# Kernel optimization log

Measured on AMD Instinct MI355X. Metric: run time of the kernel, lower is better.

The kernel has to match this reference:

```python
import jax, jax.numpy as jnp
import numpy as np

HEADS = 16
HEAD_DIM = 128
K = 128  # sparsek_k; k_actual = min(K, seq_len) = K here


def _sparsek_impl(scores):
    # scores: [B, H, S]; sparsemax-like projection with mass k
    n = scores.shape[-1]
    s = -jnp.sort(-scores, axis=-1)                      # descending sort
    cs = jnp.cumsum(s, axis=-1)
    ar = jnp.arange(1, n + 1, dtype=scores.dtype)
    thr = (cs - float(K)) / ar
    support = s > thr
    rho = jnp.clip(support.sum(axis=-1, keepdims=True), 1, None)  # int
    tau = (jnp.take_along_axis(cs, rho - 1, axis=-1) - float(K)) / rho.astype(scores.dtype)
    return jnp.clip(scores - tau, 0.0, None)


@jax.custom_vjp
def sparsek(scores):
    return _sparsek_impl(scores)


def _sparsek_fwd(scores):
    out = _sparsek_impl(scores)
    return out, (out,)


def _sparsek_bwd(res, g):
    (out,) = res
    support = (out > 0).astype(g.dtype)
    ns = jnp.clip(support.sum(axis=-1, keepdims=True), 1.0, None)
    grad = support * (g - (g * support).sum(axis=-1, keepdims=True) / ns)
    return (grad,)


sparsek.defvjp(_sparsek_fwd, _sparsek_bwd)


def setup_inputs() -> dict:
    key = jax.random.key(0)
    ks = jax.random.split(key, 9)
    B, S, H = 2, 4096, 2048
    sc = 0.02
    return {
        "x": jax.random.normal(ks[0], (B, S, H), jnp.float32),
        "wq": jax.random.normal(ks[1], (H, H), jnp.float32) * sc,
        "wk": jax.random.normal(ks[2], (H, H), jnp.float32) * sc,
        "wv": jax.random.normal(ks[3], (H, H), jnp.float32) * sc,
        "wo": jax.random.normal(ks[4], (H, H), jnp.float32) * sc,
        "sw1": jax.random.normal(ks[5], (HEAD_DIM, HEAD_DIM), jnp.float32) * sc,
        "sb1": jnp.zeros((HEAD_DIM,), jnp.float32),
        "sw2": jax.random.normal(ks[6], (1, HEAD_DIM), jnp.float32) * sc,
        "sb2": jnp.zeros((1,), jnp.float32),
    }


def reference(x, wq, wk, wv, wo, sw1, sb1, sw2, sb2):
    B, S, H = x.shape
    scale = 1.0 / np.sqrt(HEAD_DIM)

    def split_heads(y):  # [B,S,H] -> [B,heads,S,head_dim]
        return y.reshape(B, S, HEADS, HEAD_DIM).transpose(0, 2, 1, 3)

    q = split_heads(x @ wq.T)
    k = split_heads(x @ wk.T)
    v = split_heads(x @ wv.T)

    # score_net: Linear -> ReLU -> Linear(.,1), applied to keys
    kv_scores = (jax.nn.relu(k @ sw1.T + sb1) @ sw2.T + sb2)[..., 0]  # [B,heads,S]
    selection = sparsek(kv_scores)
    _, top_idx = jax.lax.top_k(selection, K)  # [B,heads,K]

    idx = top_idx[..., None]  # [B,heads,K,1]
    k_sel = jnp.take_along_axis(k, idx, axis=2)  # [B,heads,K,head_dim]
    v_sel = jnp.take_along_axis(v, idx, axis=2)

    scores = jnp.einsum('bhqd,bhkd->bhqk', q, k_sel) * scale
    attn = jax.nn.softmax(scores, axis=-1)  # dropout p=0 (eval)
    out = jnp.einsum('bhqk,bhkd->bhqd', attn, v_sel)
    out = out.transpose(0, 2, 1, 3).reshape(B, S, H)
    return out @ wo.T
```

## Files before the change

### kernel.cpp

```cpp
#include <hip/hip_runtime.h>

#define SEQ   4096
#define NB    2
#define NH    16
#define HD    128
#define TOPK  128
#define MDIM  (NB*SEQ)
#define NDIM  2048
#define KDIM  2048

typedef unsigned short u16;
typedef __bf16  v8bf __attribute__((ext_vector_type(8)));
typedef float   v4f  __attribute__((ext_vector_type(4)));

__device__ __forceinline__ u16 f2b(float f) {
    unsigned u = __float_as_uint(f);
    return (u16)((u + 0x7fffu + ((u >> 16) & 1u)) >> 16);
}
__device__ __forceinline__ float b2f(u16 h) {
    return __uint_as_float(((unsigned)h) << 16);
}

#define ASYNC16(gsrc, ldst) \
    __builtin_amdgcn_global_load_lds( \
        (const __attribute__((address_space(1))) unsigned int*)(gsrc), \
        (__attribute__((address_space(3))) unsigned int*)(ldst), 16, 0, 0)

__global__ __launch_bounds__(256) void split_f32(const float* __restrict__ in,
                                                 u16* __restrict__ hi,
                                                 u16* __restrict__ lo, long n)
{
    long i = ((long)blockIdx.x * 256 + threadIdx.x) * 4;
    if (i >= n) return;
    float4 v = *(const float4*)(in + i);
    float vv[4] = {v.x, v.y, v.z, v.w};
    u16 h[4], l[4];
#pragma unroll
    for (int j = 0; j < 4; ++j) {
        h[j] = f2b(vv[j]);
        l[j] = f2b(vv[j] - b2f(h[j]));
    }
    uint2 ph, pl;
    ph.x = (unsigned)h[0] | ((unsigned)h[1] << 16);
    ph.y = (unsigned)h[2] | ((unsigned)h[3] << 16);
    pl.x = (unsigned)l[0] | ((unsigned)l[1] << 16);
    pl.y = (unsigned)l[2] | ((unsigned)l[3] << 16);
    *(uint2*)(hi + i) = ph;
    *(uint2*)(lo + i) = pl;
}

__global__ __launch_bounds__(256) void cvt_bf16(const float* __restrict__ in,
                                                u16* __restrict__ outb, long n)
{
    long i = ((long)blockIdx.x * 256 + threadIdx.x) * 4;
    if (i >= n) return;
    float4 v = *(const float4*)(in + i);
    uint2 p;
    p.x = (unsigned)f2b(v.x) | ((unsigned)f2b(v.y) << 16);
    p.y = (unsigned)f2b(v.z) | ((unsigned)f2b(v.w) << 16);
    *(uint2*)(outb + i) = p;
}

#define GM_STORE_F32 0
#define GM_ACC_F32   1
#define GM_STORE_B16 2

#define BAR    __builtin_amdgcn_s_barrier()
#define LGK0   do { asm volatile("s_waitcnt lgkmcnt(0)" ::: "memory"); \
                    __builtin_amdgcn_sched_barrier(0); } while (0)
#define VMW(n) asm volatile("s_waitcnt vmcnt(" #n ")" ::: "memory")

__global__ __launch_bounds__(512, 2) void gemm256(const u16* __restrict__ A,
                                                  const u16* __restrict__ W,
                                                  float* __restrict__ Cf,
                                                  u16* __restrict__ Cb,
                                                  int mode)
{
    __shared__ __attribute__((aligned(16))) u16 S[65536];

    const int t    = threadIdx.x;
    const int swz  = (blockIdx.x & 7) * 32 + (blockIdx.x >> 3);
    const int bm   = swz >> 3, bn = swz & 7;
    const int lane = t & 63;
    const int wm   = (t >> 6) >> 2, wn = (t >> 6) & 3;
    const int mr   = lane & 15, q4 = lane >> 4;

    const int rA  = t >> 3;
    const int cc8 = ((t & 7) ^ (rA & 7)) * 8;
    const int rB  = (t >> 8) * 64 + (rA & 31);
    const u16* Agp = A + (long)(bm * 256 + rA) * KDIM + cc8;
    const u16* Wgp = W + (long)(bn * 256 + rB) * KDIM + cc8;
    u16* ldA = S +         rA * 64 + (t & 7) * 8;
    u16* ldB = S + 32768 + rB * 64 + (t & 7) * 8;

#define STAGE_A(kt, i) do { \
        const u16* g_ = Agp + (long)(i) * 64 * KDIM + (kt) * 64; \
        u16* d_ = ldA + ((kt) & 1) * 16384 + (i) * 4096; \
        ASYNC16(g_, d_); ASYNC16(g_ + 128 * KDIM, d_ + 8192); \
    } while (0)
#define STAGE_B(kt, j) do { \
        const u16* g_ = Wgp + (long)(j) * 32 * KDIM + (kt) * 64; \
        u16* d_ = ldB + ((kt) & 1) * 16384 + (j) * 2048; \
        ASYNC16(g_, d_); ASYNC16(g_ + 128 * KDIM, d_ + 8192); \
    } while (0)

    v4f acc[8][4];
#pragma unroll
    for (int a = 0; a < 8; ++a)
#pragma unroll
        for (int c = 0; c < 4; ++c)
            acc[a][c] = (v4f){0.f, 0.f, 0.f, 0.f};

    v8bf aF[4][2], bF[2][2][2];
#define LDA(b, i) do { \
        _Pragma("unroll") for (int mt = 0; mt < 4; ++mt) { \
            const int r_ = wm * 128 + (i) * 64 + mt * 16 + mr; \
            _Pragma("unroll") for (int ks = 0; ks < 2; ++ks) \
                aF[mt][ks] = *(const v8bf*)&S[(b) * 16384 + r_ * 64 + \
                                    (((ks * 4 + q4) ^ (r_ & 7)) * 8)]; \
        } } while (0)
#define LDB(b, j) do { \
        _Pragma("unroll") for (int nt = 0; nt < 2; ++nt) { \
            const int r_ = wn * 64 + (j) * 32 + nt * 16 + mr; \
            _Pragma("unroll") for (int ks = 0; ks < 2; ++ks) \
                bF[j][nt][ks] = *(const v8bf*)&S[32768 + (b) * 16384 + r_ * 64 + \
                                    (((ks * 4 + q4) ^ (r_ & 7)) * 8)]; \
        } } while (0)
#define MMA(i, j) do { \
        __builtin_amdgcn_s_setprio(1); \
        _Pragma("unroll") for (int mt = 0; mt < 4; ++mt) \
        _Pragma("unroll") for (int nt = 0; nt < 2; ++nt) \
        _Pragma("unroll") for (int ks = 0; ks < 2; ++ks) \
            acc[(i) * 4 + mt][(j) * 2 + nt] = \
                __builtin_amdgcn_mfma_f32_16x16x32_bf16(aF[mt][ks], bF[j][nt][ks], \
                    acc[(i) * 4 + mt][(j) * 2 + nt], 0, 0, 0); \
        __builtin_amdgcn_s_setprio(0); \
    } while (0)

    STAGE_A(0, 0); STAGE_B(0, 0); STAGE_A(0, 1); STAGE_B(0, 1);
    STAGE_A(1, 0); STAGE_B(1, 0);
    VMW(4); BAR;

    for (int it = 0; it < KDIM / 128 - 1; ++it) {
        const int T = 2 * it;
        LDA(0, 0); LDB(0, 0); STAGE_A(T + 1, 1);          BAR; LGK0; MMA(0, 0); BAR;
        LDB(0, 1);            STAGE_B(T + 1, 1);          BAR; LGK0; MMA(0, 1); BAR;
        LDA(0, 1);            STAGE_A(T + 2, 0);          BAR; LGK0; MMA(1, 0); BAR;
                              STAGE_B(T + 2, 0); VMW(4);  BAR;       MMA(1, 1); BAR;
        LDA(1, 0); LDB(1, 0); STAGE_A(T + 2, 1);          BAR; LGK0; MMA(0, 0); BAR;
        LDB(1, 1);            STAGE_B(T + 2, 1);          BAR; LGK0; MMA(0, 1); BAR;
        LDA(1, 1);            STAGE_A(T + 3, 0);          BAR; LGK0; MMA(1, 0); BAR;
                              STAGE_B(T + 3, 0); VMW(4);  BAR;       MMA(1, 1); BAR;
    }
    LDA(0, 0); LDB(0, 0); STAGE_A(31, 1);                 BAR; LGK0; MMA(0, 0); BAR;
    LDB(0, 1);            STAGE_B(31, 1);                 BAR; LGK0; MMA(0, 1); BAR;
    LDA(0, 1);                                            BAR; LGK0; MMA(1, 0); BAR;
                                             VMW(0);      BAR;       MMA(1, 1); BAR;
    LDA(1, 0); LDB(1, 0);                                 BAR; LGK0; MMA(0, 0); BAR;
    LDB(1, 1);                                            BAR; LGK0; MMA(0, 1); BAR;
    LDA(1, 1);                                            BAR; LGK0; MMA(1, 0); BAR;
                                                                     MMA(1, 1);

    const int colb = bn * 256 + wn * 64 + mr;
    const int rowb = bm * 256 + wm * 128 + q4 * 4;
#pragma unroll
    for (int a = 0; a < 8; ++a) {
        const int ro = (a >> 2) * 64 + (a & 3) * 16;
#pragma unroll
        for (int r = 0; r < 4; ++r) {
            const long base = (long)(rowb + ro + r) * NDIM + colb;
#pragma unroll
            for (int c = 0; c < 4; ++c) {
                const float v = acc[a][c][r];
                const long off = base + (c >> 1) * 32 + (c & 1) * 16;
                if (mode == GM_STORE_F32)      Cf[off] = v;
                else if (mode == GM_ACC_F32)   Cf[off] += v;
                else                           Cb[off] = f2b(v);
            }
        }
    }
#undef STAGE_A
#undef STAGE_B
#undef LDA
#undef LDB
#undef MMA
}

__global__ __launch_bounds__(256) void scorenet(const float* __restrict__ Kb,
                                                const float* __restrict__ sw1,
                                                const float* __restrict__ sb1,
                                                const float* __restrict__ sw2,
                                                const float* __restrict__ sb2,
                                                float* __restrict__ scores)
{
    __shared__ float As[16][128];
    __shared__ float Bs[16][128];
    __shared__ float red[128][17];
    const int t  = threadIdx.x;
    const int tx = t & 15, ty = t >> 4;
    const int bm = blockIdx.x;
    const int lr = t >> 1;
    const int lc = (t & 1) * 8;
    const float* Ap = Kb + (long)(bm * 128 + lr) * HD + lc;
    const float* Wp = sw1 + lr * HD + lc;

    float acc[8][8];
#pragma unroll
    for (int i = 0; i < 8; ++i)
#pragma unroll
        for (int j = 0; j < 8; ++j) acc[i][j] = 0.f;

    for (int k0 = 0; k0 < HD; k0 += 16) {
        float4 a0 = *(const float4*)(Ap + k0);
        float4 a1 = *(const float4*)(Ap + k0 + 4);
        float4 b0 = *(const float4*)(Wp + k0);
        float4 b1 = *(const float4*)(Wp + k0 + 4);
        __syncthreads();
        As[lc+0][lr] = a0.x; As[lc+1][lr] = a0.y; As[lc+2][lr] = a0.z; As[lc+3][lr] = a0.w;
        As[lc+4][lr] = a1.x; As[lc+5][lr] = a1.y; As[lc+6][lr] = a1.z; As[lc+7][lr] = a1.w;
        Bs[lc+0][lr] = b0.x; Bs[lc+1][lr] = b0.y; Bs[lc+2][lr] = b0.z; Bs[lc+3][lr] = b0.w;
        Bs[lc+4][lr] = b1.x; Bs[lc+5][lr] = b1.y; Bs[lc+6][lr] = b1.z; Bs[lc+7][lr] = b1.w;
        __syncthreads();
#pragma unroll
        for (int kk = 0; kk < 16; ++kk) {
            float a[8], b[8];
            *(float4*)&a[0] = *(const float4*)&As[kk][ty * 8];
            *(float4*)&a[4] = *(const float4*)&As[kk][ty * 8 + 4];
            *(float4*)&b[0] = *(const float4*)&Bs[kk][tx * 8];
            *(float4*)&b[4] = *(const float4*)&Bs[kk][tx * 8 + 4];
#pragma unroll
            for (int i = 0; i < 8; ++i)
#pragma unroll
                for (int j = 0; j < 8; ++j)
                    acc[i][j] = fmaf(a[i], b[j], acc[i][j]);
        }
    }

    float b1v[8], w2v[8];
#pragma unroll
    for (int j = 0; j < 8; ++j) {
        b1v[j] = sb1[tx * 8 + j];
        w2v[j] = sw2[tx * 8 + j];
    }
#pragma unroll
    for (int i = 0; i < 8; ++i) {
        float p = 0.f;
#pragma unroll
        for (int j = 0; j < 8; ++j)
            p += fmaxf(acc[i][j] + b1v[j], 0.f) * w2v[j];
        red[ty * 8 + i][tx] = p;
    }
    __syncthreads();
    if (t < 128) {
        float s = sb2[0];
#pragma unroll
        for (int c = 0; c < 16; ++c) s += red[t][c];
        long r = (long)bm * 128 + t;
        int b  = (int)(r >> 16);
        int si = (int)((r >> 4) & (SEQ - 1));
        int h  = (int)(r & (NH - 1));
        scores[((b * NH + h) << 12) + si] = s;
    }
}

__global__ __launch_bounds__(256) void topk_sel(const float* __restrict__ scores,
                                                int* __restrict__ sel)
{
    __shared__ unsigned keys[SEQ];
    __shared__ unsigned hist[256];
    __shared__ int scal2[2];
    __shared__ unsigned cntG;
    __shared__ unsigned short tpre[256];
    const int t  = threadIdx.x;
    const int bh = blockIdx.x;
    const float* sc = scores + (long)bh * SEQ;
    for (int i = t; i < SEQ; i += 256) {
        unsigned u = __float_as_uint(sc[i]);
        u = (u & 0x80000000u) ? ~u : (u | 0x80000000u);
        keys[i] = u;
    }
    unsigned prefix = 0;
    int rem = TOPK;
    const int i0 = t * 16;
    for (int shift = 24; shift >= 0; shift -= 8) {
        hist[t] = 0;
        __syncthreads();
        const unsigned pm = (shift == 24) ? 0u : (0xFFFFFFFFu << (shift + 8));
        for (int i = i0; i < i0 + 16; ++i) {
            unsigned k = keys[i];
            if (((k ^ prefix) & pm) == 0) atomicAdd(&hist[(k >> shift) & 255], 1u);
        }
        __syncthreads();
        if (t == 0) {
            int r = rem, chosen = 0;
            for (int b = 255; b >= 0; --b) {
                int c = (int)hist[b];
                if (c >= r) { chosen = b; break; }
                r -= c;
            }
            scal2[0] = chosen; scal2[1] = r;
        }
        __syncthreads();
        prefix |= ((unsigned)scal2[0]) << shift;
        rem = scal2[1];
        __syncthreads();
    }
    if (t == 0) cntG = 0;
    __syncthreads();
    const unsigned T = prefix;
    int myT = 0;
    for (int i = i0; i < i0 + 16; ++i) {
        unsigned k = keys[i];
        if (k > T) {
            unsigned p = atomicAdd(&cntG, 1u);
            sel[bh * TOPK + p] = i;
        } else if (k == T) myT++;
    }
    tpre[t] = (unsigned short)myT;
    __syncthreads();
    if (t == 0) {
        unsigned s = 0;
        for (int i = 0; i < 256; ++i) { unsigned c = tpre[i]; tpre[i] = (unsigned short)s; s += c; }
    }
    __syncthreads();
    const int base = TOPK - rem;
    int rank = tpre[t];
    for (int i = i0; i < i0 + 16; ++i) {
        if (keys[i] == T) {
            if (rank < rem) sel[bh * TOPK + base + rank] = i;
            rank++;
        }
    }
}

__global__ void gather_kv(const float* __restrict__ Kf, const u16* __restrict__ Vb,
                          const int* __restrict__ sel,
                          u16* __restrict__ ksb, u16* __restrict__ vsT)
{
    int bh = blockIdx.x >> 7;
    int j  = blockIdx.x & 127;
    int d  = threadIdx.x;
    int s  = sel[bh * TOPK + j];
    int b = bh >> 4, h = bh & (NH - 1);
    long src = ((long)(b * SEQ + s)) * NDIM + h * HD + d;
    ksb[((long)bh * TOPK + j) * HD + d] = f2b(Kf[src]);
    vsT[((long)bh * HD + d) * TOPK + j] = Vb[src];
}

__device__ __forceinline__ int paddr(int row, int col) {
    int chunk = (col >> 3) ^ (row & 15);
    return row * 128 + chunk * 8 + (col & 7);
}

__global__ __launch_bounds__(256) void attn_mfma(const u16* __restrict__ Qb,
                                                 const u16* __restrict__ ksb,
                                                 const u16* __restrict__ vsT,
                                                 u16* __restrict__ outp)
{
    __shared__ __attribute__((aligned(16))) u16 P[128 * 128];
    const int bh = blockIdx.x, qt = blockIdx.y;
    const int b = bh >> 4, h = bh & (NH - 1);
    const int t = threadIdx.x, lane = t & 63, w = t >> 6;
    const int mr = lane & 15, q4 = lane >> 4;
    const float scale = 0.08838834764831845f;

    const u16* q0p = Qb + ((long)(b * SEQ + qt * 128 + w * 32 + mr)) * NDIM
                        + h * HD + q4 * 8;
    v8bf aq[2][4];
#pragma unroll
    for (int ks = 0; ks < 4; ++ks) {
        aq[0][ks] = *(const v8bf*)(q0p + ks * 32);
        aq[1][ks] = *(const v8bf*)(q0p + 16 * NDIM + ks * 32);
    }

    const u16* kbase = ksb + (long)bh * TOPK * HD + mr * HD + q4 * 8;
    v4f acc[2][8];
#pragma unroll
    for (int i = 0; i < 2; ++i)
#pragma unroll
        for (int j = 0; j < 8; ++j) {
            acc[i][j][0] = 0.f; acc[i][j][1] = 0.f;
            acc[i][j][2] = 0.f; acc[i][j][3] = 0.f;
        }
#pragma unroll
    for (int ks = 0; ks < 4; ++ks) {
        v8bf bk[8];
#pragma unroll
        for (int nt = 0; nt < 8; ++nt)
            bk[nt] = *(const v8bf*)(kbase + (long)nt * 16 * HD + ks * 32);
#pragma unroll
        for (int mt = 0; mt < 2; ++mt)
#pragma unroll
            for (int nt = 0; nt < 8; ++nt)
                acc[mt][nt] = __builtin_amdgcn_mfma_f32_16x16x32_bf16(
                                  aq[mt][ks], bk[nt], acc[mt][nt], 0, 0, 0);
    }

#pragma unroll
    for (int mt = 0; mt < 2; ++mt)
#pragma unroll
        for (int r = 0; r < 4; ++r) {
            float mx = acc[mt][0][r];
#pragma unroll
            for (int nt = 1; nt < 8; ++nt) mx = fmaxf(mx, acc[mt][nt][r]);
#pragma unroll
            for (int m = 1; m < 16; m <<= 1) mx = fmaxf(mx, __shfl_xor(mx, m));
            float sum = 0.f;
#pragma unroll
            for (int nt = 0; nt < 8; ++nt) {
                float e = __expf((acc[mt][nt][r] - mx) * scale);
                acc[mt][nt][r] = e; sum += e;
            }
#pragma unroll
            for (int m = 1; m < 16; m <<= 1) sum += __shfl_xor(sum, m);
            float inv = 1.f / sum;
#pragma unroll
            for (int nt = 0; nt < 8; ++nt) acc[mt][nt][r] *= inv;
        }

#pragma unroll
    for (int mt = 0; mt < 2; ++mt)
#pragma unroll
        for (int nt = 0; nt < 8; ++nt)
#pragma unroll
            for (int r = 0; r < 4; ++r)
                P[paddr(w * 32 + mt * 16 + q4 * 4 + r, nt * 16 + mr)] =
                    f2b(acc[mt][nt][r]);
    __syncthreads();

    const u16* vbase = vsT + (long)bh * HD * TOPK + mr * TOPK + q4 * 8;
    v4f acc2[2][8];
#pragma unroll
    for (int i = 0; i < 2; ++i)
#pragma unroll
        for (int j = 0; j < 8; ++j) {
            acc2[i][j][0] = 0.f; acc2[i][j][1] = 0.f;
            acc2[i][j][2] = 0.f; acc2[i][j][3] = 0.f;
        }
#pragma unroll
    for (int ks = 0; ks < 4; ++ks) {
        v8bf ap[2];
        ap[0] = *(const v8bf*)&P[paddr(w * 32 + mr,      ks * 32 + q4 * 8)];
        ap[1] = *(const v8bf*)&P[paddr(w * 32 + 16 + mr, ks * 32 + q4 * 8)];
        v8bf bv[8];
#pragma unroll
        for (int nt = 0; nt < 8; ++nt)
            bv[nt] = *(const v8bf*)(vbase + (long)nt * 16 * TOPK + ks * 32);
#pragma unroll
        for (int mt = 0; mt < 2; ++mt)
#pragma unroll
            for (int nt = 0; nt < 8; ++nt)
                acc2[mt][nt] = __builtin_amdgcn_mfma_f32_16x16x32_bf16(
                                   ap[mt], bv[nt], acc2[mt][nt], 0, 0, 0);
    }
    __syncthreads();

#pragma unroll
    for (int mt = 0; mt < 2; ++mt)
#pragma unroll
        for (int nt = 0; nt < 8; ++nt)
#pragma unroll
            for (int r = 0; r < 4; ++r)
                P[paddr(w * 32 + mt * 16 + q4 * 4 + r, nt * 16 + mr)] =
                    f2b(acc2[mt][nt][r]);
    __syncthreads();

    u16* obase = outp + ((long)(b * SEQ + qt * 128)) * NDIM + h * HD;
    for (int f = t; f < 2048; f += 256) {
        int row = f >> 4, cc = f & 15;
        uint4 val = *(const uint4*)&P[row * 128 + (cc ^ (row & 15)) * 8];
        *(uint4*)(obase + (long)row * NDIM + cc * 8) = val;
    }
}

extern "C" void kernel_launch(void* const* d_in, const int* in_sizes, int n_in,
                              void* d_out, int out_size, void* d_ws, size_t ws_size,
                              hipStream_t stream)
{
    const float* x   = (const float*)d_in[0];
    const float* wq  = (const float*)d_in[1];
    const float* wk  = (const float*)d_in[2];
    const float* wv  = (const float*)d_in[3];
    const float* wo  = (const float*)d_in[4];
    const float* sw1 = (const float*)d_in[5];
    const float* sb1 = (const float*)d_in[6];
    const float* sw2 = (const float*)d_in[7];
    const float* sb2 = (const float*)d_in[8];
    float* out = (float*)d_out;

    char* base = (char*)d_ws;
    u16*   xh      = (u16*)  base;
    u16*   xl      = (u16*) (base + 33554432L);
    float* Kf      = (float*)(base + 67108864L);
    u16*   Vb      = (u16*) (base + 134217728L);
    u16*   W1      = (u16*) (base + 167772160L);
    u16*   W2      = (u16*) (base + 176160768L);
    float* scoresB = (float*)(base + 184549376L);
    int*   sel     = (int*) (base + 185073664L);
    u16*   ksb     = (u16*) (base + 185090048L);
    u16*   vsT     = (u16*) (base + 186138624L);
    u16*   Qb      = xl;
    u16*   AOb     = Vb;

    const long NX = (long)MDIM * NDIM;
    dim3 blk(256);
    const int g256 = (MDIM / 256) * (NDIM / 256);

    split_f32<<<16384, blk, 0, stream>>>(x,  xh, xl, NX);
    split_f32<<<4096,  blk, 0, stream>>>(wk, W1, W2, (long)NDIM * KDIM);
    gemm256<<<g256, 512, 0, stream>>>(xh, W1, Kf, nullptr, GM_STORE_F32);
    gemm256<<<g256, 512, 0, stream>>>(xh, W2, Kf, nullptr, GM_ACC_F32);
    gemm256<<<g256, 512, 0, stream>>>(xl, W1, Kf, nullptr, GM_ACC_F32);
    cvt_bf16<<<4096, blk, 0, stream>>>(wq, W1, (long)NDIM * KDIM);
    cvt_bf16<<<4096, blk, 0, stream>>>(wv, W2, (long)NDIM * KDIM);
    gemm256<<<g256, 512, 0, stream>>>(xh, W1, nullptr, Qb, GM_STORE_B16);
    gemm256<<<g256, 512, 0, stream>>>(xh, W2, nullptr, Vb, GM_STORE_B16);
    scorenet<<<(MDIM * NH) / 128, blk, 0, stream>>>(Kf, sw1, sb1, sw2, sb2, scoresB);
    topk_sel<<<NB * NH, blk, 0, stream>>>(scoresB, sel);
    gather_kv<<<NB * NH * TOPK, 128, 0, stream>>>(Kf, Vb, sel, ksb, vsT);
    attn_mfma<<<dim3(NB * NH, SEQ / 128), blk, 0, stream>>>(Qb, ksb, vsT, AOb);
    cvt_bf16<<<4096, blk, 0, stream>>>(wo, W1, (long)NDIM * KDIM);
    gemm256<<<g256, 512, 0, stream>>>(AOb, W1, out, nullptr, GM_STORE_F32);
}
```

Before: 739.8 us.

## Fuse three split-bf16 K-projection GEMMs into one kernel; split LDS waits

```diff
diff --git a/kernel.cpp b/kernel.cpp
--- a/kernel.cpp
+++ b/kernel.cpp
@@ -26,6 +26,14 @@
         (const __attribute__((address_space(1))) unsigned int*)(gsrc), \
         (__attribute__((address_space(3))) unsigned int*)(ldst), 16, 0, 0)
 
+#define BAR     __builtin_amdgcn_s_barrier()
+#define SCB0    __builtin_amdgcn_sched_barrier(0)
+#define SP1     __builtin_amdgcn_s_setprio(1)
+#define SP0     __builtin_amdgcn_s_setprio(0)
+#define LGKC(n) do { asm volatile("s_waitcnt lgkmcnt(" #n ")" ::: "memory"); \
+                     __builtin_amdgcn_sched_barrier(0); } while (0)
+#define VMW(n)  asm volatile("s_waitcnt vmcnt(" #n ")" ::: "memory")
+
 __global__ __launch_bounds__(256) void split_f32(const float* __restrict__ in,
                                                  u16* __restrict__ hi,
                                                  u16* __restrict__ lo, long n)
@@ -64,11 +72,6 @@
 #define GM_STORE_F32 0
 #define GM_ACC_F32   1
 #define GM_STORE_B16 2
-
-#define BAR    __builtin_amdgcn_s_barrier()
-#define LGK0   do { asm volatile("s_waitcnt lgkmcnt(0)" ::: "memory"); \
-                    __builtin_amdgcn_sched_barrier(0); } while (0)
-#define VMW(n) asm volatile("s_waitcnt vmcnt(" #n ")" ::: "memory")
 
 __global__ __launch_bounds__(512, 2) void gemm256(const u16* __restrict__ A,
                                                   const u16* __restrict__ W,
@@ -112,29 +115,27 @@
             acc[a][c] = (v4f){0.f, 0.f, 0.f, 0.f};
 
     v8bf aF[4][2], bF[2][2][2];
-#define LDA(b, i) do { \
-        _Pragma("unroll") for (int mt = 0; mt < 4; ++mt) { \
-            const int r_ = wm * 128 + (i) * 64 + mt * 16 + mr; \
-            _Pragma("unroll") for (int ks = 0; ks < 2; ++ks) \
-                aF[mt][ks] = *(const v8bf*)&S[(b) * 16384 + r_ * 64 + \
-                                    (((ks * 4 + q4) ^ (r_ & 7)) * 8)]; \
-        } } while (0)
 #define LDB(b, j) do { \
         _Pragma("unroll") for (int nt = 0; nt < 2; ++nt) { \
             const int r_ = wn * 64 + (j) * 32 + nt * 16 + mr; \
             _Pragma("unroll") for (int ks = 0; ks < 2; ++ks) \
                 bF[j][nt][ks] = *(const v8bf*)&S[32768 + (b) * 16384 + r_ * 64 + \
                                     (((ks * 4 + q4) ^ (r_ & 7)) * 8)]; \
-        } } while (0)
-#define MMA(i, j) do { \
-        __builtin_amdgcn_s_setprio(1); \
-        _Pragma("unroll") for (int mt = 0; mt < 4; ++mt) \
+        } SCB0; } while (0)
+#define LDAH(b, i, h) do { \
+        _Pragma("unroll") for (int mt = 2*(h); mt < 2*(h)+2; ++mt) { \
+            const int r_ = wm * 128 + (i) * 64 + mt * 16 + mr; \
+            _Pragma("unroll") for (int ks = 0; ks < 2; ++ks) \
+                aF[mt][ks] = *(const v8bf*)&S[(b) * 16384 + r_ * 64 + \
+                                    (((ks * 4 + q4) ^ (r_ & 7)) * 8)]; \
+        } SCB0; } while (0)
+#define MMAH(i, j, h) do { \
+        _Pragma("unroll") for (int mt = 2*(h); mt < 2*(h)+2; ++mt) \
         _Pragma("unroll") for (int nt = 0; nt < 2; ++nt) \
         _Pragma("unroll") for (int ks = 0; ks < 2; ++ks) \
             acc[(i) * 4 + mt][(j) * 2 + nt] = \
-                __builtin_amdgcn_mfma_f32_16x16x32_bf16(aF[mt][ks], bF[j][nt][ks], \
+                __builtin_amdgcn_mfma_f32_16x16x32_bf16(aF[mt][ks], bF[(j)][nt][ks], \
                     acc[(i) * 4 + mt][(j) * 2 + nt], 0, 0, 0); \
-        __builtin_amdgcn_s_setprio(0); \
     } while (0)
 
     STAGE_A(0, 0); STAGE_B(0, 0); STAGE_A(0, 1); STAGE_B(0, 1);
@@ -143,23 +144,38 @@
 
     for (int it = 0; it < KDIM / 128 - 1; ++it) {
         const int T = 2 * it;
-        LDA(0, 0); LDB(0, 0); STAGE_A(T + 1, 1);          BAR; LGK0; MMA(0, 0); BAR;
-        LDB(0, 1);            STAGE_B(T + 1, 1);          BAR; LGK0; MMA(0, 1); BAR;
-        LDA(0, 1);            STAGE_A(T + 2, 0);          BAR; LGK0; MMA(1, 0); BAR;
-                              STAGE_B(T + 2, 0); VMW(4);  BAR;       MMA(1, 1); BAR;
-        LDA(1, 0); LDB(1, 0); STAGE_A(T + 2, 1);          BAR; LGK0; MMA(0, 0); BAR;
-        LDB(1, 1);            STAGE_B(T + 2, 1);          BAR; LGK0; MMA(0, 1); BAR;
-        LDA(1, 1);            STAGE_A(T + 3, 0);          BAR; LGK0; MMA(1, 0); BAR;
-                              STAGE_B(T + 3, 0); VMW(4);  BAR;       MMA(1, 1); BAR;
-    }
-    LDA(0, 0); LDB(0, 0); STAGE_A(31, 1);                 BAR; LGK0; MMA(0, 0); BAR;
-    LDB(0, 1);            STAGE_B(31, 1);                 BAR; LGK0; MMA(0, 1); BAR;
-    LDA(0, 1);                                            BAR; LGK0; MMA(1, 0); BAR;
-                                             VMW(0);      BAR;       MMA(1, 1); BAR;
-    LDA(1, 0); LDB(1, 0);                                 BAR; LGK0; MMA(0, 0); BAR;
-    LDB(1, 1);                                            BAR; LGK0; MMA(0, 1); BAR;
-    LDA(1, 1);                                            BAR; LGK0; MMA(1, 0); BAR;
-                                                                     MMA(1, 1);
+        LDB(0,0); LDAH(0,0,0); LDAH(0,0,1); STAGE_A(T+1,1);
+        BAR; LGKC(4); SP1; MMAH(0,0,0); LGKC(0); MMAH(0,0,1); SP0; BAR;
+        LDB(0,1); STAGE_B(T+1,1);
+        BAR; LGKC(0); SP1; MMAH(0,1,0); MMAH(0,1,1); SP0; BAR;
+        LDAH(0,1,0); LDAH(0,1,1); STAGE_A(T+2,0);
+        BAR; LGKC(4); SP1; MMAH(1,0,0); LGKC(0); MMAH(1,0,1); SP0; BAR;
+        STAGE_B(T+2,0); VMW(4);
+        BAR; SP1; MMAH(1,1,0); MMAH(1,1,1); SP0; BAR;
+        LDB(1,0); LDAH(1,0,0); LDAH(1,0,1); STAGE_A(T+2,1);
+        BAR; LGKC(4); SP1; MMAH(0,0,0); LGKC(0); MMAH(0,0,1); SP0; BAR;
+        LDB(1,1); STAGE_B(T+2,1);
+        BAR; LGKC(0); SP1; MMAH(0,1,0); MMAH(0,1,1); SP0; BAR;
+        LDAH(1,1,0); LDAH(1,1,1); STAGE_A(T+3,0);
+        BAR; LGKC(4); SP1; MMAH(1,0,0); LGKC(0); MMAH(1,0,1); SP0; BAR;
+        STAGE_B(T+3,0); VMW(4);
+        BAR; SP1; MMAH(1,1,0); MMAH(1,1,1); SP0; BAR;
+    }
+    LDB(0,0); LDAH(0,0,0); LDAH(0,0,1); STAGE_A(31,1);
+    BAR; LGKC(4); SP1; MMAH(0,0,0); LGKC(0); MMAH(0,0,1); SP0; BAR;
+    LDB(0,1); STAGE_B(31,1);
+    BAR; LGKC(0); SP1; MMAH(0,1,0); MMAH(0,1,1); SP0; BAR;
+    LDAH(0,1,0); LDAH(0,1,1);
+    BAR; LGKC(4); SP1; MMAH(1,0,0); LGKC(0); MMAH(1,0,1); SP0; BAR;
+    VMW(0);
+    BAR; SP1; MMAH(1,1,0); MMAH(1,1,1); SP0; BAR;
+    LDB(1,0); LDAH(1,0,0); LDAH(1,0,1);
+    BAR; LGKC(4); SP1; MMAH(0,0,0); LGKC(0); MMAH(0,0,1); SP0; BAR;
+    LDB(1,1);
+    BAR; LGKC(0); SP1; MMAH(0,1,0); MMAH(0,1,1); SP0; BAR;
+    LDAH(1,1,0); LDAH(1,1,1);
+    BAR; LGKC(4); SP1; MMAH(1,0,0); LGKC(0); MMAH(1,0,1); SP0; BAR;
+    SP1; MMAH(1,1,0); MMAH(1,1,1); SP0;
 
     const int colb = bn * 256 + wn * 64 + mr;
     const int rowb = bm * 256 + wm * 128 + q4 * 4;
@@ -181,9 +197,125 @@
     }
 #undef STAGE_A
 #undef STAGE_B
-#undef LDA
 #undef LDB
-#undef MMA
+#undef LDAH
+#undef MMAH
+}
+
+__global__ __launch_bounds__(512, 2) void gemm_k3(const u16* __restrict__ Ah,
+                                                  const u16* __restrict__ Al,
+                                                  const u16* __restrict__ W1,
+                                                  const u16* __restrict__ W2,
+                                                  float* __restrict__ Cf)
+{
+    __shared__ __attribute__((aligned(16))) u16 S[65536];
+
+    const int t    = threadIdx.x;
+    const int swz  = (blockIdx.x & 7) * 32 + (blockIdx.x >> 3);
+    const int bm   = swz >> 3, bn = swz & 7;
+    const int lane = t & 63;
+    const int wm   = (t >> 6) >> 2, wn = (t >> 6) & 3;
+    const int mr   = lane & 15, q4 = lane >> 4;
+    const int ck   = q4 ^ ((mr ^ (mr >> 2)) & 3);
+
+    const int lr    = t >> 2;
+    const int cks   = (t & 3) ^ ((lr ^ (lr >> 2)) & 3);
+    const int growA = (lr & 63) + ((lr & 64) << 1);
+    const int growB = (lr & 31) + ((lr >> 5) << 6);
+    const u16* Ahp = Ah + (long)(bm * 256 + growA) * KDIM + cks * 8;
+    const u16* Alp = Al + (long)(bm * 256 + growA) * KDIM + cks * 8;
+    const u16* W1p = W1 + (long)(bn * 256 + growB) * KDIM + cks * 8;
+    const u16* W2p = W2 + (long)(bn * 256 + growB) * KDIM + cks * 8;
+    u16* dA = S +         lr * 32 + (t & 3) * 8;
+    u16* dB = S + 16384 + lr * 32 + (t & 3) * 8;
+
+#define K3SA(kt, s) do { \
+        const long g_ = (long)(s) * 64 * KDIM + (kt) * 32; \
+        u16* d_ = dA + (((kt) & 1) << 15) + (s) * 8192; \
+        ASYNC16(Ahp + g_, d_); ASYNC16(Alp + g_, d_ + 4096); } while (0)
+#define K3SB(kt, s) do { \
+        const long g_ = (long)(s) * 32 * KDIM + (kt) * 32; \
+        u16* d_ = dB + (((kt) & 1) << 15) + (s) * 8192; \
+        ASYNC16(W1p + g_, d_); ASYNC16(W2p + g_, d_ + 4096); } while (0)
+
+    v4f acc[8][4];
+#pragma unroll
+    for (int a = 0; a < 8; ++a)
+#pragma unroll
+        for (int c = 0; c < 4; ++c)
+            acc[a][c] = (v4f){0.f, 0.f, 0.f, 0.f};
+
+    v8bf aFh[4], aFl[4], b1[2][2], b2[2][2];
+    const int aBase = wm * 2048 + mr * 32 + ck * 8;
+    const int bBase = 16384 + wn * 1024 + mr * 32 + ck * 8;
+
+#define K3RB(bb, j) do { \
+        _Pragma("unroll") for (int nt = 0; nt < 2; ++nt) { \
+            b1[j][nt] = *(const v8bf*)&S[(bb) + bBase + (j) * 8192 + nt * 512]; \
+            b2[j][nt] = *(const v8bf*)&S[(bb) + bBase + (j) * 8192 + nt * 512 + 4096]; \
+        } SCB0; } while (0)
+#define K3RAH(bb, i) do { _Pragma("unroll") for (int mt = 0; mt < 4; ++mt) \
+        aFh[mt] = *(const v8bf*)&S[(bb) + aBase + (i) * 8192 + mt * 512]; SCB0; } while (0)
+#define K3RAL(bb, i) do { _Pragma("unroll") for (int mt = 0; mt < 4; ++mt) \
+        aFl[mt] = *(const v8bf*)&S[(bb) + aBase + (i) * 8192 + mt * 512 + 4096]; SCB0; } while (0)
+#define K3CL(af, bx, i, j) do { \
+        _Pragma("unroll") for (int mt = 0; mt < 4; ++mt) \
+        _Pragma("unroll") for (int nt = 0; nt < 2; ++nt) \
+            acc[(i) * 4 + mt][(j) * 2 + nt] = __builtin_amdgcn_mfma_f32_16x16x32_bf16( \
+                af[mt], bx[(j)][nt], acc[(i) * 4 + mt][(j) * 2 + nt], 0, 0, 0); } while (0)
+
+    K3SA(0, 0); K3SB(0, 0); K3SB(0, 1); K3SA(0, 1);
+    VMW(4); BAR;
+
+    for (int T = 0; T < KDIM / 32 - 1; ++T) {
+        const int bb = (T & 1) << 15;
+        K3RB(bb, 0); K3RAH(bb, 0); K3RAL(bb, 0); K3SA(T + 1, 0);
+        BAR; LGKC(4); SP1; K3CL(aFh, b1, 0, 0); K3CL(aFh, b2, 0, 0);
+        LGKC(0); K3CL(aFl, b1, 0, 0); SP0; VMW(4); BAR;
+        K3RB(bb, 1); K3SB(T + 1, 0);
+        BAR; LGKC(0); SP1; K3CL(aFh, b1, 0, 1); K3CL(aFh, b2, 0, 1);
+        K3CL(aFl, b1, 0, 1); SP0; VMW(4); BAR;
+        K3RAH(bb, 1); K3RAL(bb, 1); K3SB(T + 1, 1);
+        BAR; LGKC(4); SP1; K3CL(aFh, b1, 1, 0); K3CL(aFh, b2, 1, 0);
+        LGKC(0); K3CL(aFl, b1, 1, 0); SP0; BAR;
+        K3SA(T + 1, 1);
+        BAR; SP1; K3CL(aFh, b1, 1, 1); K3CL(aFh, b2, 1, 1);
+        K3CL(aFl, b1, 1, 1); SP0; VMW(4); BAR;
+    }
+    {
+        const int bb = 32768;
+        K3RB(bb, 0); K3RAH(bb, 0); K3RAL(bb, 0);
+        BAR; LGKC(4); SP1; K3CL(aFh, b1, 0, 0); K3CL(aFh, b2, 0, 0);
+        LGKC(0); K3CL(aFl, b1, 0, 0); SP0; VMW(2); BAR;
+        K3RB(bb, 1);
+        BAR; LGKC(0); SP1; K3CL(aFh, b1, 0, 1); K3CL(aFh, b2, 0, 1);
+        K3CL(aFl, b1, 0, 1); SP0; VMW(0); BAR;
+        K3RAH(bb, 1); K3RAL(bb, 1);
+        BAR; LGKC(4); SP1; K3CL(aFh, b1, 1, 0); K3CL(aFh, b2, 1, 0);
+        LGKC(0); K3CL(aFl, b1, 1, 0); SP0; BAR;
+        SP1; K3CL(aFh, b1, 1, 1); K3CL(aFh, b2, 1, 1);
+        K3CL(aFl, b1, 1, 1); SP0;
+    }
+
+    const int colb = bn * 256 + wn * 64 + mr;
+    const int rowb = bm * 256 + wm * 128 + q4 * 4;
+#pragma unroll
+    for (int a = 0; a < 8; ++a) {
+        const int ro = (a >> 2) * 64 + (a & 3) * 16;
+#pragma unroll
+        for (int r = 0; r < 4; ++r) {
+            const long base = (long)(rowb + ro + r) * NDIM + colb;
+#pragma unroll
+            for (int c = 0; c < 4; ++c)
+                Cf[base + (c >> 1) * 32 + (c & 1) * 16] = acc[a][c][r];
+        }
+    }
+#undef K3SA
+#undef K3SB
+#undef K3RB
+#undef K3RAH
+#undef K3RAL
+#undef K3CL
 }
 
 __global__ __launch_bounds__(256) void scorenet(const float* __restrict__ Kb,
@@ -508,9 +640,7 @@
 
     split_f32<<<16384, blk, 0, stream>>>(x,  xh, xl, NX);
     split_f32<<<4096,  blk, 0, stream>>>(wk, W1, W2, (long)NDIM * KDIM);
-    gemm256<<<g256, 512, 0, stream>>>(xh, W1, Kf, nullptr, GM_STORE_F32);
-    gemm256<<<g256, 512, 0, stream>>>(xh, W2, Kf, nullptr, GM_ACC_F32);
-    gemm256<<<g256, 512, 0, stream>>>(xl, W1, Kf, nullptr, GM_ACC_F32);
+    gemm_k3<<<g256, 512, 0, stream>>>(xh, xl, W1, W2, Kf);
     cvt_bf16<<<4096, blk, 0, stream>>>(wq, W1, (long)NDIM * KDIM);
     cvt_bf16<<<4096, blk, 0, stream>>>(wv, W2, (long)NDIM * KDIM);
     gemm256<<<g256, 512, 0, stream>>>(xh, W1, nullptr, Qb, GM_STORE_B16);
```

New measurement: 667.0 us. 9.8% less time.

## Fuse three-pass split-bf16 K projection into one GEMM and repipeline gemm256

Applied to the files above, without the earlier changes.

```diff
diff --git a/kernel.cpp b/kernel.cpp
--- a/kernel.cpp
+++ b/kernel.cpp
@@ -26,6 +26,13 @@
         (const __attribute__((address_space(1))) unsigned int*)(gsrc), \
         (__attribute__((address_space(3))) unsigned int*)(ldst), 16, 0, 0)
 
+#define SCB0    __builtin_amdgcn_sched_barrier(0)
+#define BARS    do { __builtin_amdgcn_s_barrier(); SCB0; } while (0)
+#define SP1     __builtin_amdgcn_s_setprio(1)
+#define SP0     __builtin_amdgcn_s_setprio(0)
+#define LGKC(n) do { asm volatile("s_waitcnt lgkmcnt(" #n ")" ::: "memory"); SCB0; } while (0)
+#define VMW(n)  do { asm volatile("s_waitcnt vmcnt(" #n ")" ::: "memory"); SCB0; } while (0)
+
 __global__ __launch_bounds__(256) void split_f32(const float* __restrict__ in,
                                                  u16* __restrict__ hi,
                                                  u16* __restrict__ lo, long n)
@@ -65,11 +72,6 @@
 #define GM_ACC_F32   1
 #define GM_STORE_B16 2
 
-#define BAR    __builtin_amdgcn_s_barrier()
-#define LGK0   do { asm volatile("s_waitcnt lgkmcnt(0)" ::: "memory"); \
-                    __builtin_amdgcn_sched_barrier(0); } while (0)
-#define VMW(n) asm volatile("s_waitcnt vmcnt(" #n ")" ::: "memory")
-
 __global__ __launch_bounds__(512, 2) void gemm256(const u16* __restrict__ A,
                                                   const u16* __restrict__ W,
                                                   float* __restrict__ Cf,
@@ -84,6 +86,7 @@
     const int lane = t & 63;
     const int wm   = (t >> 6) >> 2, wn = (t >> 6) & 3;
     const int mr   = lane & 15, q4 = lane >> 4;
+    const int sl0  = (q4 ^ (mr & 7)) * 8, sl1 = sl0 ^ 32;
 
     const int rA  = t >> 3;
     const int cc8 = ((t & 7) ^ (rA & 7)) * 8;
@@ -93,16 +96,14 @@
     u16* ldA = S +         rA * 64 + (t & 7) * 8;
     u16* ldB = S + 32768 + rB * 64 + (t & 7) * 8;
 
-#define STAGE_A(kt, i) do { \
+#define STAGE_A(kt, i) { \
         const u16* g_ = Agp + (long)(i) * 64 * KDIM + (kt) * 64; \
         u16* d_ = ldA + ((kt) & 1) * 16384 + (i) * 4096; \
-        ASYNC16(g_, d_); ASYNC16(g_ + 128 * KDIM, d_ + 8192); \
-    } while (0)
-#define STAGE_B(kt, j) do { \
+        ASYNC16(g_, d_); ASYNC16(g_ + 128 * KDIM, d_ + 8192); }
+#define STAGE_B(kt, j) { \
         const u16* g_ = Wgp + (long)(j) * 32 * KDIM + (kt) * 64; \
         u16* d_ = ldB + ((kt) & 1) * 16384 + (j) * 2048; \
-        ASYNC16(g_, d_); ASYNC16(g_ + 128 * KDIM, d_ + 8192); \
-    } while (0)
+        ASYNC16(g_, d_); ASYNC16(g_ + 128 * KDIM, d_ + 8192); }
 
     v4f acc[8][4];
 #pragma unroll
@@ -111,55 +112,50 @@
         for (int c = 0; c < 4; ++c)
             acc[a][c] = (v4f){0.f, 0.f, 0.f, 0.f};
 
-    v8bf aF[4][2], bF[2][2][2];
-#define LDA(b, i) do { \
-        _Pragma("unroll") for (int mt = 0; mt < 4; ++mt) { \
-            const int r_ = wm * 128 + (i) * 64 + mt * 16 + mr; \
-            _Pragma("unroll") for (int ks = 0; ks < 2; ++ks) \
-                aF[mt][ks] = *(const v8bf*)&S[(b) * 16384 + r_ * 64 + \
-                                    (((ks * 4 + q4) ^ (r_ & 7)) * 8)]; \
-        } } while (0)
-#define LDB(b, j) do { \
-        _Pragma("unroll") for (int nt = 0; nt < 2; ++nt) { \
-            const int r_ = wn * 64 + (j) * 32 + nt * 16 + mr; \
-            _Pragma("unroll") for (int ks = 0; ks < 2; ++ks) \
-                bF[j][nt][ks] = *(const v8bf*)&S[32768 + (b) * 16384 + r_ * 64 + \
-                                    (((ks * 4 + q4) ^ (r_ & 7)) * 8)]; \
-        } } while (0)
-#define MMA(i, j) do { \
-        __builtin_amdgcn_s_setprio(1); \
+    v8bf Aa[4][2], Ab[4][2];
+    v8bf Ba[2][2], Bb[2][2];
+
+#define RD_A(dst, b, i) { _Pragma("unroll") for (int mt = 0; mt < 4; ++mt) { \
+        const int ro_ = (b) * 16384 + (wm * 128 + (i) * 64 + mt * 16 + mr) * 64; \
+        dst[mt][0] = *(const v8bf*)&S[ro_ + sl0]; \
+        dst[mt][1] = *(const v8bf*)&S[ro_ + sl1]; } }
+#define RD_B(dst, b, j) { _Pragma("unroll") for (int nt = 0; nt < 2; ++nt) { \
+        const int ro_ = 32768 + (b) * 16384 + (wn * 64 + (j) * 32 + nt * 16 + mr) * 64; \
+        dst[nt][0] = *(const v8bf*)&S[ro_ + sl0]; \
+        dst[nt][1] = *(const v8bf*)&S[ro_ + sl1]; } }
+#define MM(AH, il, BH, jl) { SP1; \
         _Pragma("unroll") for (int mt = 0; mt < 4; ++mt) \
         _Pragma("unroll") for (int nt = 0; nt < 2; ++nt) \
         _Pragma("unroll") for (int ks = 0; ks < 2; ++ks) \
-            acc[(i) * 4 + mt][(j) * 2 + nt] = \
-                __builtin_amdgcn_mfma_f32_16x16x32_bf16(aF[mt][ks], bF[j][nt][ks], \
-                    acc[(i) * 4 + mt][(j) * 2 + nt], 0, 0, 0); \
-        __builtin_amdgcn_s_setprio(0); \
-    } while (0)
-
-    STAGE_A(0, 0); STAGE_B(0, 0); STAGE_A(0, 1); STAGE_B(0, 1);
-    STAGE_A(1, 0); STAGE_B(1, 0);
-    VMW(4); BAR;
-
-    for (int it = 0; it < KDIM / 128 - 1; ++it) {
-        const int T = 2 * it;
-        LDA(0, 0); LDB(0, 0); STAGE_A(T + 1, 1);          BAR; LGK0; MMA(0, 0); BAR;
-        LDB(0, 1);            STAGE_B(T + 1, 1);          BAR; LGK0; MMA(0, 1); BAR;
-        LDA(0, 1);            STAGE_A(T + 2, 0);          BAR; LGK0; MMA(1, 0); BAR;
-                              STAGE_B(T + 2, 0); VMW(4);  BAR;       MMA(1, 1); BAR;
-        LDA(1, 0); LDB(1, 0); STAGE_A(T + 2, 1);          BAR; LGK0; MMA(0, 0); BAR;
-        LDB(1, 1);            STAGE_B(T + 2, 1);          BAR; LGK0; MMA(0, 1); BAR;
-        LDA(1, 1);            STAGE_A(T + 3, 0);          BAR; LGK0; MMA(1, 0); BAR;
-                              STAGE_B(T + 3, 0); VMW(4);  BAR;       MMA(1, 1); BAR;
-    }
-    LDA(0, 0); LDB(0, 0); STAGE_A(31, 1);                 BAR; LGK0; MMA(0, 0); BAR;
-    LDB(0, 1);            STAGE_B(31, 1);                 BAR; LGK0; MMA(0, 1); BAR;
-    LDA(0, 1);                                            BAR; LGK0; MMA(1, 0); BAR;
-                                             VMW(0);      BAR;       MMA(1, 1); BAR;
-    LDA(1, 0); LDB(1, 0);                                 BAR; LGK0; MMA(0, 0); BAR;
-    LDB(1, 1);                                            BAR; LGK0; MMA(0, 1); BAR;
-    LDA(1, 1);                                            BAR; LGK0; MMA(1, 0); BAR;
-                                                                     MMA(1, 1);
+            acc[4*(il)+mt][2*(jl)+nt] = __builtin_amdgcn_mfma_f32_16x16x32_bf16( \
+                AH[mt][ks], BH[nt][ks], acc[4*(il)+mt][2*(jl)+nt], 0, 0, 0); \
+        SP0; }
+
+#define G_EV(U) \
+    RD_B(Bb, 0, 1); RD_A(Ab, 0, 1); SCB0; LGKC(12); MM(Aa, 0, Ba, 0); BARS; \
+    STAGE_A((U)+2, 0); STAGE_B((U)+2, 0); SCB0; VMW(8); LGKC(8); MM(Aa, 0, Bb, 1); BARS; \
+    RD_A(Aa, 1, 0); SCB0; STAGE_B((U)+2, 1); LGKC(8); MM(Ab, 1, Bb, 1); BARS; \
+    RD_B(Bb, 1, 0); SCB0; STAGE_A((U)+2, 1); VMW(8); MM(Ab, 1, Ba, 0); BARS;
+#define G_OD(U) \
+    RD_B(Ba, 1, 1); RD_A(Ab, 1, 1); SCB0; LGKC(12); MM(Aa, 0, Bb, 0); BARS; \
+    STAGE_A((U)+2, 0); STAGE_B((U)+2, 0); SCB0; VMW(8); LGKC(8); MM(Aa, 0, Ba, 1); BARS; \
+    RD_A(Aa, 0, 0); SCB0; STAGE_B((U)+2, 1); LGKC(8); MM(Ab, 1, Ba, 1); BARS; \
+    RD_B(Ba, 0, 0); SCB0; STAGE_A((U)+2, 1); VMW(8); MM(Ab, 1, Bb, 0); BARS;
+
+    STAGE_A(0, 0); STAGE_B(0, 0); STAGE_B(0, 1); STAGE_A(0, 1);
+    STAGE_A(1, 0); STAGE_B(1, 0); STAGE_B(1, 1); STAGE_A(1, 1);
+    VMW(8); BARS;
+    RD_A(Aa, 0, 0); RD_B(Ba, 0, 0); SCB0;
+
+    for (int U = 0; U < KDIM / 64 - 2; U += 2) { G_EV(U); G_OD(U + 1); }
+    RD_B(Bb, 0, 1); RD_A(Ab, 0, 1); SCB0; LGKC(12); MM(Aa, 0, Ba, 0); BARS;
+    VMW(4); LGKC(8); MM(Aa, 0, Bb, 1); BARS;
+    RD_A(Aa, 1, 0); SCB0; LGKC(8); MM(Ab, 1, Bb, 1); BARS;
+    RD_B(Bb, 1, 0); SCB0; VMW(0); MM(Ab, 1, Ba, 0); BARS;
+    RD_B(Ba, 1, 1); RD_A(Ab, 1, 1); SCB0; LGKC(12); MM(Aa, 0, Bb, 0); BARS;
+    LGKC(8); MM(Aa, 0, Ba, 1); BARS;
+    LGKC(0); MM(Ab, 1, Ba, 1);
+    MM(Ab, 1, Bb, 0);
 
     const int colb = bn * 256 + wn * 64 + mr;
     const int rowb = bm * 256 + wm * 128 + q4 * 4;
@@ -181,9 +177,125 @@
     }
 #undef STAGE_A
 #undef STAGE_B
-#undef LDA
-#undef LDB
-#undef MMA
+#undef RD_A
+#undef RD_B
+#undef MM
+#undef G_EV
+#undef G_OD
+}
+
+__global__ __launch_bounds__(512, 2) void gemm_k3(const u16* __restrict__ Ah,
+                                                  const u16* __restrict__ Al,
+                                                  const u16* __restrict__ W1,
+                                                  const u16* __restrict__ W2,
+                                                  float* __restrict__ Cf)
+{
+    __shared__ __attribute__((aligned(16))) u16 S[65536];
+
+    const int t    = threadIdx.x;
+    const int swz  = (blockIdx.x & 7) * 32 + (blockIdx.x >> 3);
+    const int bm   = swz >> 3, bn = swz & 7;
+    const int lane = t & 63;
+    const int wm   = (t >> 6) >> 2, wn = (t >> 6) & 3;
+    const int mr   = lane & 15, q4 = lane >> 4;
+    const int sl0  = (q4 ^ (mr & 7)) * 8, sl1 = sl0 ^ 32;
+    const int rlB0 = (wn & 1) * 32 + (wn >> 1) * 64 + mr;
+
+    const int lsl  = (t & 7) ^ ((t >> 3) & 7);
+    const int cS   = (lsl & 3) * 8;
+    const u16* baseA = ((lsl < 4) ? Ah : Al)
+                     + (long)(bm * 256 + (t >> 3)) * KDIM + cS;
+    const u16* baseB = ((lsl < 4) ? W1 : W2)
+                     + (long)(bn * 256 + (t >> 8) * 64 + ((t >> 3) & 31)) * KDIM + cS;
+    u16* dA = S +         t * 8;
+    u16* dB = S + 32768 + t * 8;
+
+#define K_SA(kt, si) { \
+        ASYNC16(baseA + ((long)(si) * 64      ) * KDIM + (kt) * 32, \
+                dA + (((kt) & 1) << 14) + (si) * 8192); \
+        ASYNC16(baseA + ((long)(si) * 64 + 128) * KDIM + (kt) * 32, \
+                dA + (((kt) & 1) << 14) + (si) * 8192 + 4096); }
+#define K_SB(kt, si) { \
+        ASYNC16(baseB + ((long)(si) * 32      ) * KDIM + (kt) * 32, \
+                dB + (((kt) & 1) << 14) + (si) * 8192); \
+        ASYNC16(baseB + ((long)(si) * 32 + 128) * KDIM + (kt) * 32, \
+                dB + (((kt) & 1) << 14) + (si) * 8192 + 4096); }
+
+    v4f acc[8][4];
+#pragma unroll
+    for (int a = 0; a < 8; ++a)
+#pragma unroll
+        for (int c = 0; c < 4; ++c)
+            acc[a][c] = (v4f){0.f, 0.f, 0.f, 0.f};
+
+    v8bf Ha[4], La[4], Hb[4], Lb[4];
+    v8bf B1a[2], B2a[2], B1b[2], B2b[2];
+
+#define K_RDA(dh, dl, b, i) { _Pragma("unroll") for (int mt = 0; mt < 4; ++mt) { \
+        const int ad = (b) * 16384 + (i) * 8192 + (mt * 16 + wm * 64 + mr) * 64; \
+        dh[mt] = *(const v8bf*)&S[ad + sl0]; \
+        dl[mt] = *(const v8bf*)&S[ad + sl1]; } }
+#define K_RDB(d1, d2, b, j) { _Pragma("unroll") for (int u = 0; u < 2; ++u) { \
+        const int ad = 32768 + (b) * 16384 + (j) * 8192 + (u * 16 + rlB0) * 64; \
+        d1[u] = *(const v8bf*)&S[ad + sl0]; \
+        d2[u] = *(const v8bf*)&S[ad + sl1]; } }
+#define K_MM(H, L, il, Bx, By, jl) { SP1; \
+        _Pragma("unroll") for (int mt = 0; mt < 4; ++mt) \
+        _Pragma("unroll") for (int u = 0; u < 2; ++u) { \
+            acc[4*(il)+mt][2*(jl)+u] = __builtin_amdgcn_mfma_f32_16x16x32_bf16( \
+                H[mt], Bx[u], acc[4*(il)+mt][2*(jl)+u], 0, 0, 0); \
+            acc[4*(il)+mt][2*(jl)+u] = __builtin_amdgcn_mfma_f32_16x16x32_bf16( \
+                H[mt], By[u], acc[4*(il)+mt][2*(jl)+u], 0, 0, 0); \
+            acc[4*(il)+mt][2*(jl)+u] = __builtin_amdgcn_mfma_f32_16x16x32_bf16( \
+                L[mt], Bx[u], acc[4*(il)+mt][2*(jl)+u], 0, 0, 0); } \
+        SP0; }
+
+#define K_EV(U) \
+    K_RDB(B1b, B2b, 0, 1); K_RDA(Hb, Lb, 0, 1); SCB0; LGKC(12); K_MM(Ha, La, 0, B1a, B2a, 0); BARS; \
+    K_SA((U)+2, 0); K_SB((U)+2, 0); SCB0; VMW(8); LGKC(8); K_MM(Ha, La, 0, B1b, B2b, 1); BARS; \
+    K_RDA(Ha, La, 1, 0); SCB0; K_SB((U)+2, 1); LGKC(8); K_MM(Hb, Lb, 1, B1b, B2b, 1); BARS; \
+    K_RDB(B1b, B2b, 1, 0); SCB0; K_SA((U)+2, 1); VMW(8); K_MM(Hb, Lb, 1, B1a, B2a, 0); BARS;
+#define K_OD(U) \
+    K_RDB(B1a, B2a, 1, 1); K_RDA(Hb, Lb, 1, 1); SCB0; LGKC(12); K_MM(Ha, La, 0, B1b, B2b, 0); BARS; \
+    K_SA((U)+2, 0); K_SB((U)+2, 0); SCB0; VMW(8); LGKC(8); K_MM(Ha, La, 0, B1a, B2a, 1); BARS; \
+    K_RDA(Ha, La, 0, 0); SCB0; K_SB((U)+2, 1); LGKC(8); K_MM(Hb, Lb, 1, B1a, B2a, 1); BARS; \
+    K_RDB(B1a, B2a, 0, 0); SCB0; K_SA((U)+2, 1); VMW(8); K_MM(Hb, Lb, 1, B1b, B2b, 0); BARS;
+
+    K_SA(0, 0); K_SB(0, 0); K_SB(0, 1); K_SA(0, 1);
+    K_SA(1, 0); K_SB(1, 0); K_SB(1, 1); K_SA(1, 1);
+    VMW(8); BARS;
+    K_RDA(Ha, La, 0, 0); K_RDB(B1a, B2a, 0, 0); SCB0;
+
+    for (int U = 0; U < KDIM / 32 - 2; U += 2) { K_EV(U); K_OD(U + 1); }
+    K_RDB(B1b, B2b, 0, 1); K_RDA(Hb, Lb, 0, 1); SCB0; LGKC(12); K_MM(Ha, La, 0, B1a, B2a, 0); BARS;
+    VMW(4); LGKC(8); K_MM(Ha, La, 0, B1b, B2b, 1); BARS;
+    K_RDA(Ha, La, 1, 0); SCB0; LGKC(8); K_MM(Hb, Lb, 1, B1b, B2b, 1); BARS;
+    K_RDB(B1b, B2b, 1, 0); SCB0; VMW(0); K_MM(Hb, Lb, 1, B1a, B2a, 0); BARS;
+    K_RDB(B1a, B2a, 1, 1); K_RDA(Hb, Lb, 1, 1); SCB0; LGKC(12); K_MM(Ha, La, 0, B1b, B2b, 0); BARS;
+    LGKC(8); K_MM(Ha, La, 0, B1a, B2a, 1); BARS;
+    LGKC(0); K_MM(Hb, Lb, 1, B1a, B2a, 1);
+    K_MM(Hb, Lb, 1, B1b, B2b, 0);
+
+    const int colb = bn * 256 + wn * 64 + mr;
+    const int rowb = bm * 256 + wm * 128 + q4 * 4;
+#pragma unroll
+    for (int a = 0; a < 8; ++a) {
+        const int ro = (a >> 2) * 64 + (a & 3) * 16;
+#pragma unroll
+        for (int r = 0; r < 4; ++r) {
+            const long base = (long)(rowb + ro + r) * NDIM + colb;
+#pragma unroll
+            for (int c = 0; c < 4; ++c)
+                Cf[base + (c >> 1) * 32 + (c & 1) * 16] = acc[a][c][r];
+        }
+    }
+#undef K_SA
+#undef K_SB
+#undef K_RDA
+#undef K_RDB
+#undef K_MM
+#undef K_EV
+#undef K_OD
 }
 
 __global__ __launch_bounds__(256) void scorenet(const float* __restrict__ Kb,
@@ -508,9 +620,7 @@
 
     split_f32<<<16384, blk, 0, stream>>>(x,  xh, xl, NX);
     split_f32<<<4096,  blk, 0, stream>>>(wk, W1, W2, (long)NDIM * KDIM);
-    gemm256<<<g256, 512, 0, stream>>>(xh, W1, Kf, nullptr, GM_STORE_F32);
-    gemm256<<<g256, 512, 0, stream>>>(xh, W2, Kf, nullptr, GM_ACC_F32);
-    gemm256<<<g256, 512, 0, stream>>>(xl, W1, Kf, nullptr, GM_ACC_F32);
+    gemm_k3<<<g256, 512, 0, stream>>>(xh, xl, W1, W2, Kf);
     cvt_bf16<<<4096, blk, 0, stream>>>(wq, W1, (long)NDIM * KDIM);
     cvt_bf16<<<4096, blk, 0, stream>>>(wv, W2, (long)NDIM * KDIM);
     gemm256<<<g256, 512, 0, stream>>>(xh, W1, nullptr, Qb, GM_STORE_B16);
```

New measurement: 787.1 us. 6.4% more time.
